# Kernel tuning notes

Hardware: AMD Instinct MI355X
Metric: run time of the kernel (lower is better)

The kernel has to match this reference:

```python
import jax, jax.numpy as jnp
import numpy as np

N = 50000
E = 400000
D = 128

def _linear(v, W, b):
    return v @ W + b

def setup_inputs() -> dict:
    key = jax.random.key(0)
    ks = jax.random.split(key, 24)
    inp = {
        'h': jax.random.normal(ks[0], (N, D), jnp.float32),
        'x': jax.random.normal(ks[1], (N, 3), jnp.float32),
        'src': jax.random.randint(ks[2], (E,), 0, N, jnp.int32),
        'dst': jax.random.randint(ks[3], (E,), 0, N, jnp.int32),
        'distances': jax.random.uniform(ks[4], (E,), jnp.float32),
        'bpp_bias': jax.random.uniform(ks[5], (E,), jnp.float32),
        'msa_bias': jax.random.uniform(ks[6], (E,), jnp.float32),
        'chem_bias': jax.random.uniform(ks[7], (E,), jnp.float32),
        'relative_offset': jax.random.normal(ks[8], (E,), jnp.float32),
        'chain_break_mask': jax.random.uniform(ks[9], (E,), jnp.float32),
    }
    s = 0.05
    # weights stored [in, out] (transpose of torch Linear)
    inp['msg_W1'] = jax.random.normal(ks[10], (2 * D + 6, D), jnp.float32) * s
    inp['msg_b1'] = jnp.zeros((D,), jnp.float32)
    inp['msg_W2'] = jax.random.normal(ks[11], (D, D), jnp.float32) * s
    inp['msg_b2'] = jnp.zeros((D,), jnp.float32)
    inp['h_W1'] = jax.random.normal(ks[12], (2 * D, D), jnp.float32) * s
    inp['h_b1'] = jnp.zeros((D,), jnp.float32)
    inp['h_W2'] = jax.random.normal(ks[13], (D, D), jnp.float32) * s
    inp['h_b2'] = jnp.zeros((D,), jnp.float32)
    inp['c_W1'] = jax.random.normal(ks[14], (D, D), jnp.float32) * s
    inp['c_b1'] = jnp.zeros((D,), jnp.float32)
    inp['c_W2'] = jax.random.normal(ks[15], (D, 1), jnp.float32) * s
    inp['c_b2'] = jnp.zeros((1,), jnp.float32)
    return inp

def reference(h, x, src, dst, distances, bpp_bias, msa_bias, chem_bias,
              relative_offset, chain_break_mask,
              msg_W1, msg_b1, msg_W2, msg_b2,
              h_W1, h_b1, h_W2, h_b2,
              c_W1, c_b1, c_W2, c_b2):
    n = h.shape[0]
    h_src = h[src]                      # [E, D]
    h_dst = h[dst]                      # [E, D]
    diff = x[src] - x[dst]              # [E, 3]
    dist2 = (distances * distances)[:, None]
    feat = jnp.concatenate([
        h_src, h_dst, dist2,
        bpp_bias[:, None], msa_bias[:, None], chem_bias[:, None],
        relative_offset[:, None], chain_break_mask[:, None]], axis=-1)  # [E, 2D+6]
    m_ij = jax.nn.silu(_linear(jax.nn.silu(_linear(feat, msg_W1, msg_b1)), msg_W2, msg_b2))  # [E, D]
    counts = jax.ops.segment_sum(jnp.ones((src.shape[0],), h.dtype), src, num_segments=n)[:, None]  # [N,1]
    denom = jnp.maximum(counts, 1.0)
    m_i = jax.ops.segment_sum(m_ij, src, num_segments=n) / denom      # [N, D]
    h_out = h + _linear(jax.nn.silu(_linear(jnp.concatenate([h, m_i], -1), h_W1, h_b1)), h_W2, h_b2)
    coef = jnp.tanh(_linear(jax.nn.silu(_linear(m_ij, c_W1, c_b1)), c_W2, c_b2))  # [E, 1]
    delta = jax.ops.segment_sum(diff * coef, src, num_segments=n) / denom          # [N, 3]
    x_out = x + delta
    return h_out, x_out
```

## Files before the change

kernel.cpp:

```cpp
#include <hip/hip_runtime.h>
#include <hip/hip_bf16.h>

typedef short bf16x8 __attribute__((ext_vector_type(8)));
typedef float f32x16 __attribute__((ext_vector_type(16)));
typedef int   i32x4v __attribute__((ext_vector_type(4)));
typedef unsigned u32;

#define MFMA32(a,b,c) __builtin_amdgcn_mfma_f32_32x32x16_bf16((a),(b),(c),0,0,0)

__device__ __forceinline__ u32 pkbf(float x, float y) {
  union { u32 u; __hip_bfloat16 h[2]; } t;
  t.h[0] = __float2bfloat16(x);
  t.h[1] = __float2bfloat16(y);
  return t.u;
}
__device__ __forceinline__ float bf2f(u32 lo16) {
  union { u32 u; float f; } t; t.u = lo16 << 16; return t.f;
}
__device__ __forceinline__ float silu_f(float v) { return v / (1.f + __expf(-v)); }
__device__ __forceinline__ float tanh_f(float v) {
  float e = __expf(2.f * fabsf(v));
  float t = 1.f - 2.f / (e + 1.f);
  return copysignf(t, v);
}

template<int NT>
__device__ __forceinline__ void stage_w128t(const float* __restrict__ W, short* wA, int tid) {
  for (int p = tid; p < 8192; p += NT) {
    int j = p & 127;
    int k = (p >> 7) << 1;
    u32 u = pkbf(W[k * 128 + j], W[k * 128 + 128 + j]);
    int off = j * 256 + (((k >> 3) ^ (j & 15)) << 4) + ((k & 7) << 1);
    *(u32*)((char*)wA + off) = u;
  }
}
__device__ __forceinline__ bf16x8 ldsA(const short* wA, int j, int kbase) {
  int off = j * 256 + (((kbase >> 3) ^ (j & 15)) << 4);
  return __builtin_bit_cast(bf16x8, *(const i32x4v*)((const char*)wA + off));
}

__device__ __forceinline__ void row_chunks(u32 p0, u32 p1, u32 p2, u32 p3,
                                           u32 p4, u32 p5, u32 p6, u32 p7,
                                           int hi, char* rowptr, int jm) {
  u32 x0 = (u32)__shfl_xor((int)(hi ? p0 : p4), 32);
  u32 x1 = (u32)__shfl_xor((int)(hi ? p1 : p5), 32);
  u32 x2 = (u32)__shfl_xor((int)(hi ? p2 : p6), 32);
  u32 x3 = (u32)__shfl_xor((int)(hi ? p3 : p7), 32);
  i32x4v c0, c1;
  if (hi) {
    c0[0] = (int)x0; c0[1] = (int)x1; c0[2] = (int)p4; c0[3] = (int)p5;
    c1[0] = (int)x2; c1[1] = (int)x3; c1[2] = (int)p6; c1[3] = (int)p7;
  } else {
    c0[0] = (int)p0; c0[1] = (int)p1; c0[2] = (int)x0; c0[3] = (int)x1;
    c1[0] = (int)p2; c1[1] = (int)p3; c1[2] = (int)x2; c1[3] = (int)x3;
  }
  *(i32x4v*)(rowptr + jm * 64 + hi * 32)      = c0;
  *(i32x4v*)(rowptr + jm * 64 + hi * 32 + 16) = c1;
}

__device__ __forceinline__ void trans_store1(const f32x16& a, const float* bias, int hi,
                                             char* rowptr, bool va, int jm) {
  float v[16];
  #pragma unroll
  for (int r = 0; r < 16; ++r) {
    int rowloc = (r & 3) + 8 * (r >> 2) + 4 * hi;
    v[r] = silu_f(a[r] + bias[jm * 32 + rowloc]);
  }
  u32 p0 = pkbf(v[0], v[1]),  p1 = pkbf(v[2], v[3]);
  u32 p2 = pkbf(v[4], v[5]),  p3 = pkbf(v[6], v[7]);
  u32 p4 = pkbf(v[8], v[9]),  p5 = pkbf(v[10], v[11]);
  u32 p6 = pkbf(v[12], v[13]), p7 = pkbf(v[14], v[15]);
  if (va) row_chunks(p0, p1, p2, p3, p4, p5, p6, p7, hi, rowptr, jm);
}

__device__ __forceinline__ void trans_frag1(const f32x16& a, const float* bias, int hi,
                                            i32x4v* fr, char* rowptr, bool va, int jm) {
  float v[16];
  #pragma unroll
  for (int r = 0; r < 16; ++r) {
    int rowloc = (r & 3) + 8 * (r >> 2) + 4 * hi;
    v[r] = silu_f(a[r] + bias[jm * 32 + rowloc]);
  }
  u32 p0 = pkbf(v[0], v[1]),  p1 = pkbf(v[2], v[3]);
  u32 p2 = pkbf(v[4], v[5]),  p3 = pkbf(v[6], v[7]);
  u32 p4 = pkbf(v[8], v[9]),  p5 = pkbf(v[10], v[11]);
  u32 p6 = pkbf(v[12], v[13]), p7 = pkbf(v[14], v[15]);
  {
    u32 g1 = (u32)__shfl_xor((int)(hi ? p0 : p2), 32);
    u32 g2 = (u32)__shfl_xor((int)(hi ? p1 : p3), 32);
    i32x4v w;
    w[0] = hi ? (int)g1 : (int)p0;
    w[1] = hi ? (int)g2 : (int)p1;
    w[2] = hi ? (int)p2 : (int)g1;
    w[3] = hi ? (int)p3 : (int)g2;
    fr[jm * 2] = w;
    u32 g1b = (u32)__shfl_xor((int)(hi ? p4 : p6), 32);
    u32 g2b = (u32)__shfl_xor((int)(hi ? p5 : p7), 32);
    i32x4v w2;
    w2[0] = hi ? (int)g1b : (int)p4;
    w2[1] = hi ? (int)g2b : (int)p5;
    w2[2] = hi ? (int)p6 : (int)g1b;
    w2[3] = hi ? (int)p7 : (int)g2b;
    fr[jm * 2 + 1] = w2;
  }
  if (va) row_chunks(p0, p1, p2, p3, p4, p5, p6, p7, hi, rowptr, jm);
}


__global__ void kconv(const float* __restrict__ h, char* __restrict__ hbf, int total16) {
  int i = blockIdx.x * 256 + threadIdx.x;
  if (i >= total16) return;
  const float4* h4 = (const float4*)h;
  float4 a = h4[(size_t)i * 2], b = h4[(size_t)i * 2 + 1];
  i32x4v w;
  w[0] = (int)pkbf(a.x, a.y); w[1] = (int)pkbf(a.z, a.w);
  w[2] = (int)pkbf(b.x, b.y); w[3] = (int)pkbf(b.z, b.w);
  *(i32x4v*)(hbf + (size_t)i * 16) = w;
}

__global__ void khist(const int* __restrict__ src, int* __restrict__ cnt, int E) {
  int e = blockIdx.x * 256 + threadIdx.x;
  if (e < E) atomicAdd(&cnt[src[e]], 1);
}

__global__ void kscan1(const int* __restrict__ cnt, int* __restrict__ part,
                       int* __restrict__ bsums, int N) {
  __shared__ int sh[1024];
  int tid = threadIdx.x, i = blockIdx.x * 1024 + tid;
  int v = (i < N) ? cnt[i] : 0;
  sh[tid] = v; __syncthreads();
  for (int off = 1; off < 1024; off <<= 1) {
    int t = (tid >= off) ? sh[tid - off] : 0;
    __syncthreads();
    sh[tid] += t;
    __syncthreads();
  }
  if (i < N) part[i] = sh[tid] - v;
  if (tid == 1023) bsums[blockIdx.x] = sh[1023];
}

__global__ void kscan2(int* __restrict__ bsums, int nb) {
  __shared__ int sh[64];
  int tid = threadIdx.x;
  int v = (tid < nb) ? bsums[tid] : 0;
  sh[tid] = v; __syncthreads();
  for (int off = 1; off < 64; off <<= 1) {
    int t = (tid >= off) ? sh[tid - off] : 0;
    __syncthreads();
    sh[tid] += t;
    __syncthreads();
  }
  if (tid < nb) bsums[tid] = sh[tid] - v;
}

__global__ void kscan3(const int* __restrict__ bsums, int* __restrict__ part,
                       int* __restrict__ head, int N) {
  int i = blockIdx.x * 1024 + threadIdx.x;
  if (i < N) {
    int v = part[i] + bsums[blockIdx.x];
    part[i] = v;
    head[i] = v;
  }
}

__global__ void kscatter(const int* __restrict__ src, const int* __restrict__ dst,
                         const float* __restrict__ dist, const float* __restrict__ bpp,
                         const float* __restrict__ msa, const float* __restrict__ chem,
                         const float* __restrict__ rel, const float* __restrict__ cbm,
                         int* __restrict__ head, int* __restrict__ rec, int E) {
  int e = blockIdx.x * 256 + threadIdx.x;
  if (e >= E) return;
  int s = src[e];
  int p = atomicAdd(&head[s], 1);
  float q = dist[e];
  i32x4v a;
  a[0] = s;
  a[1] = dst[e];
  a[2] = (int)pkbf(q * q, bpp[e]);
  a[3] = (int)pkbf(msa[e], chem[e]);
  *(i32x4v*)(rec + (size_t)p * 8) = a;
  rec[(size_t)p * 8 + 4] = (int)pkbf(rel[e], cbm[e]);
}

__global__ __launch_bounds__(512, 2)
void kedgeA(const char* __restrict__ hbf, const int* __restrict__ rec,
            const float* __restrict__ mW1, const float* __restrict__ mb1,
            char* __restrict__ t1, int E)
{
  __shared__ short wA0[16384], wA1[16384];
  __shared__ short wE[2048];
  __shared__ float sb1[128];

  const int tid = threadIdx.x, wid = tid >> 6, lane = tid & 63;
  const int col = lane & 31, hi = lane >> 5;

  stage_w128t<512>(mW1, wA0, tid);
  stage_w128t<512>(mW1 + 16384, wA1, tid);
  for (int p = tid; p < 2048; p += 512) {
    int j = p >> 4, kk = p & 15;
    float w = (kk < 6) ? mW1[(256 + kk) * 128 + j] : 0.f;
    wE[j * 16 + kk] = (short)(pkbf(w, 0.f) & 0xffffu);
  }
  if (tid < 128) sb1[tid] = mb1[tid];
  __syncthreads();

  const int T = (E + 31) / 32;
  const int stride = gridDim.x * 8;
  int t = blockIdx.x * 8 + wid;
  if (t >= T) return;

  int p = t * 32 + col;
  int pc = p < E ? p : E - 1;
  i32x4v ra = *(const i32x4v*)(rec + (size_t)pc * 8);
  int ev2 = rec[(size_t)pc * 8 + 4];

  while (t < T) {
    bool va = p < E;
    int s = ra[0], d = ra[1];

    i32x4v bs[8], bd[8];
    #pragma unroll
    for (int kc = 0; kc < 8; ++kc)
      bs[kc] = *(const i32x4v*)(hbf + (size_t)s * 256 + kc * 32 + hi * 16);
    #pragma unroll
    for (int kc = 0; kc < 8; ++kc)
      bd[kc] = *(const i32x4v*)(hbf + (size_t)d * 256 + kc * 32 + hi * 16);

    int tn = t + stride;
    int pn = tn * 32 + col;
    int pcn = pn < E ? pn : E - 1;
    i32x4v nra = *(const i32x4v*)(rec + (size_t)pcn * 8);
    int nev2 = rec[(size_t)pcn * 8 + 4];

    char* rowptr = t1 + (size_t)p * 256;
    #pragma unroll
    for (int g = 0; g < 2; ++g) {
      f32x16 acc2[2];
      #pragma unroll
      for (int j2 = 0; j2 < 2; ++j2)
        #pragma unroll
        for (int r = 0; r < 16; ++r) acc2[j2][r] = 0.f;

      #pragma unroll
      for (int kc = 0; kc < 8; ++kc) {
        bf16x8 bb = __builtin_bit_cast(bf16x8, bs[kc]);
        #pragma unroll
        for (int j2 = 0; j2 < 2; ++j2)
          acc2[j2] = MFMA32(ldsA(wA0, (g * 2 + j2) * 32 + col, kc * 16 + hi * 8), bb, acc2[j2]);
      }
      #pragma unroll
      for (int kc = 0; kc < 8; ++kc) {
        bf16x8 bb = __builtin_bit_cast(bf16x8, bd[kc]);
        #pragma unroll
        for (int j2 = 0; j2 < 2; ++j2)
          acc2[j2] = MFMA32(ldsA(wA1, (g * 2 + j2) * 32 + col, kc * 16 + hi * 8), bb, acc2[j2]);
      }
      {
        i32x4v ev;
        ev[0] = hi ? 0 : ra[2];
        ev[1] = hi ? 0 : ra[3];
        ev[2] = hi ? 0 : ev2;
        ev[3] = 0;
        bf16x8 be = __builtin_bit_cast(bf16x8, ev);
        #pragma unroll
        for (int j2 = 0; j2 < 2; ++j2) {
          bf16x8 af = __builtin_bit_cast(bf16x8,
              *(const i32x4v*)((const char*)wE + ((g * 2 + j2) * 32 + col) * 32 + hi * 16));
          acc2[j2] = MFMA32(af, be, acc2[j2]);
        }
      }
      #pragma unroll
      for (int j2 = 0; j2 < 2; ++j2)
        trans_store1(acc2[j2], sb1, hi, rowptr, va, g * 2 + j2);
    }

    t = tn; p = pn; ra = nra; ev2 = nev2;
  }
}

__global__ __launch_bounds__(512, 2)
void kedgeB(char* buf,
            const float* __restrict__ mW2, const float* __restrict__ mb2,
            const float* __restrict__ cW1, const float* __restrict__ cb1,
            const float* __restrict__ cW2v, const float* __restrict__ cb2,
            float* __restrict__ coef, int E)
{
  __shared__ short wA2[16384], wA3[16384];
  __shared__ float sb2[128], scb1[128], scw2[128];
  __shared__ float scb2v[1];

  const int tid = threadIdx.x, wid = tid >> 6, lane = tid & 63;
  const int col = lane & 31, hi = lane >> 5;

  stage_w128t<512>(mW2, wA2, tid);
  stage_w128t<512>(cW1, wA3, tid);
  if (tid < 128) {
    sb2[tid] = mb2[tid]; scb1[tid] = cb1[tid]; scw2[tid] = cW2v[tid];
  }
  if (tid == 0) scb2v[0] = cb2[0];
  __syncthreads();

  const int T = (E + 31) / 32;
  const int stride = gridDim.x * 8;
  for (int t = blockIdx.x * 8 + wid; t < T; t += stride) {
    int p = t * 32 + col;
    bool va = p < E;
    int pc = va ? p : E - 1;

    i32x4v b[8];
    #pragma unroll
    for (int kc = 0; kc < 8; ++kc)
      b[kc] = *(const i32x4v*)(buf + (size_t)pc * 256 + kc * 32 + hi * 16);

    char* rowptr = buf + (size_t)p * 256;
    i32x4v fr[8];
    #pragma unroll
    for (int g = 0; g < 2; ++g) {
      f32x16 acc2[2];
      #pragma unroll
      for (int j2 = 0; j2 < 2; ++j2)
        #pragma unroll
        for (int r = 0; r < 16; ++r) acc2[j2][r] = 0.f;
      #pragma unroll
      for (int kc = 0; kc < 8; ++kc) {
        bf16x8 bb = __builtin_bit_cast(bf16x8, b[kc]);
        #pragma unroll
        for (int j2 = 0; j2 < 2; ++j2)
          acc2[j2] = MFMA32(ldsA(wA2, (g * 2 + j2) * 32 + col, kc * 16 + hi * 8), bb, acc2[j2]);
      }
      #pragma unroll
      for (int j2 = 0; j2 < 2; ++j2)
        trans_frag1(acc2[j2], sb2, hi, fr, rowptr, va, g * 2 + j2);
    }

    float part = 0.f;
    #pragma unroll
    for (int g = 0; g < 2; ++g) {
      f32x16 acc2[2];
      #pragma unroll
      for (int j2 = 0; j2 < 2; ++j2)
        #pragma unroll
        for (int r = 0; r < 16; ++r) acc2[j2][r] = 0.f;
      #pragma unroll
      for (int kc = 0; kc < 8; ++kc) {
        bf16x8 bb = __builtin_bit_cast(bf16x8, fr[kc]);
        #pragma unroll
        for (int j2 = 0; j2 < 2; ++j2)
          acc2[j2] = MFMA32(ldsA(wA3, (g * 2 + j2) * 32 + col, kc * 16 + hi * 8), bb, acc2[j2]);
      }
      #pragma unroll
      for (int j2 = 0; j2 < 2; ++j2) {
        int jm = g * 2 + j2;
        #pragma unroll
        for (int r = 0; r < 16; ++r) {
          int rowloc = (r & 3) + 8 * (r >> 2) + 4 * hi;
          part += silu_f(acc2[j2][r] + scb1[jm * 32 + rowloc]) * scw2[jm * 32 + rowloc];
        }
      }
    }
    part += __shfl_xor(part, 32);
    float cf = tanh_f(part + scb2v[0]);
    if (va && hi == 0) coef[p] = cf;
  }
}

__global__ __launch_bounds__(256)
void kagg(const char* __restrict__ m_ij, const int* __restrict__ row_start,
          const int* __restrict__ cnt, const float* __restrict__ coef,
          const int* __restrict__ rec, const float* __restrict__ x,
          char* __restrict__ mibf, float* __restrict__ outX, int N)
{
  int n = blockIdx.x * 16 + (threadIdx.x >> 4);
  int t = threadIdx.x & 15;
  if (n >= N) return;
  int st = row_start[n], c = cnt[n];
  float a[8] = {0.f, 0.f, 0.f, 0.f, 0.f, 0.f, 0.f, 0.f};
  for (int k = 0; k < c; ++k) {
    i32x4v u = *(const i32x4v*)(m_ij + (size_t)(st + k) * 256 + t * 16);
    #pragma unroll
    for (int q = 0; q < 4; ++q) {
      u32 w = (u32)u[q];
      a[q * 2]     += bf2f(w & 0xffffu);
      a[q * 2 + 1] += bf2f(w >> 16);
    }
  }
  float inv = 1.f / fmaxf((float)c, 1.f);
  i32x4v o;
  #pragma unroll
  for (int q = 0; q < 4; ++q) o[q] = (int)pkbf(a[q * 2] * inv, a[q * 2 + 1] * inv);
  *(i32x4v*)(mibf + (size_t)n * 256 + t * 16) = o;
  if (t == 0) {
    float x0 = x[(size_t)n * 3], x1 = x[(size_t)n * 3 + 1], x2 = x[(size_t)n * 3 + 2];
    float dx = 0.f, dy = 0.f, dz = 0.f;
    for (int k = 0; k < c; ++k) {
      float cf = coef[st + k];
      int dn = rec[(size_t)(st + k) * 8 + 1];
      dx += (x0 - x[(size_t)dn * 3])     * cf;
      dy += (x1 - x[(size_t)dn * 3 + 1]) * cf;
      dz += (x2 - x[(size_t)dn * 3 + 2]) * cf;
    }
    outX[(size_t)n * 3]     = x0 + dx * inv;
    outX[(size_t)n * 3 + 1] = x1 + dy * inv;
    outX[(size_t)n * 3 + 2] = x2 + dz * inv;
  }
}

__global__ __launch_bounds__(512, 2)
void knode1(const char* __restrict__ hbf, const char* __restrict__ mibf,
            const float* __restrict__ hW1, const float* __restrict__ hb1,
            char* __restrict__ t1h, int N)
{
  __shared__ short wA0[16384], wA1[16384];
  __shared__ float sb1[128];
  const int tid = threadIdx.x, wid = tid >> 6, lane = tid & 63;
  const int col = lane & 31, hi = lane >> 5;
  stage_w128t<512>(hW1, wA0, tid);
  stage_w128t<512>(hW1 + 16384, wA1, tid);
  if (tid < 128) sb1[tid] = hb1[tid];
  __syncthreads();

  int T = (N + 31) / 32;
  int t = blockIdx.x * 8 + wid;
  if (t >= T) return;
  int n = t * 32 + col;
  bool va = n < N;
  int nc = va ? n : N - 1;

  i32x4v bh[8], bm[8];
  #pragma unroll
  for (int kc = 0; kc < 8; ++kc)
    bh[kc] = *(const i32x4v*)(hbf + (size_t)nc * 256 + kc * 32 + hi * 16);
  #pragma unroll
  for (int kc = 0; kc < 8; ++kc)
    bm[kc] = *(const i32x4v*)(mibf + (size_t)nc * 256 + kc * 32 + hi * 16);

  char* rowptr = t1h + (size_t)n * 256;
  #pragma unroll
  for (int g = 0; g < 2; ++g) {
    f32x16 acc2[2];
    #pragma unroll
    for (int j2 = 0; j2 < 2; ++j2)
      #pragma unroll
      for (int r = 0; r < 16; ++r) acc2[j2][r] = 0.f;
    #pragma unroll
    for (int kc = 0; kc < 8; ++kc) {
      bf16x8 bb = __builtin_bit_cast(bf16x8, bh[kc]);
      #pragma unroll
      for (int j2 = 0; j2 < 2; ++j2)
        acc2[j2] = MFMA32(ldsA(wA0, (g * 2 + j2) * 32 + col, kc * 16 + hi * 8), bb, acc2[j2]);
    }
    #pragma unroll
    for (int kc = 0; kc < 8; ++kc) {
      bf16x8 bb = __builtin_bit_cast(bf16x8, bm[kc]);
      #pragma unroll
      for (int j2 = 0; j2 < 2; ++j2)
        acc2[j2] = MFMA32(ldsA(wA1, (g * 2 + j2) * 32 + col, kc * 16 + hi * 8), bb, acc2[j2]);
    }
    #pragma unroll
    for (int j2 = 0; j2 < 2; ++j2)
      trans_store1(acc2[j2], sb1, hi, rowptr, va, g * 2 + j2);
  }
}

__global__ __launch_bounds__(512, 2)
void knode2(const char* __restrict__ t1h, const float* __restrict__ hW2,
            const float* __restrict__ hb2, const float* __restrict__ h,
            float* __restrict__ outH, int N)
{
  __shared__ short wA0[16384];
  __shared__ float sb2[128];
  const int tid = threadIdx.x, wid = tid >> 6, lane = tid & 63;
  const int col = lane & 31, hi = lane >> 5;
  stage_w128t<512>(hW2, wA0, tid);
  if (tid < 128) sb2[tid] = hb2[tid];
  __syncthreads();

  int T = (N + 31) / 32;
  int t = blockIdx.x * 8 + wid;
  if (t >= T) return;
  int n = t * 32 + col;
  bool va = n < N;
  int nc = va ? n : N - 1;

  i32x4v b[8];
  #pragma unroll
  for (int kc = 0; kc < 8; ++kc)
    b[kc] = *(const i32x4v*)(t1h + (size_t)nc * 256 + kc * 32 + hi * 16);

  const float4* h4 = (const float4*)h;
  #pragma unroll
  for (int g = 0; g < 2; ++g) {
    f32x16 acc2[2];
    #pragma unroll
    for (int j2 = 0; j2 < 2; ++j2)
      #pragma unroll
      for (int r = 0; r < 16; ++r) acc2[j2][r] = 0.f;
    #pragma unroll
    for (int kc = 0; kc < 8; ++kc) {
      bf16x8 bb = __builtin_bit_cast(bf16x8, b[kc]);
      #pragma unroll
      for (int j2 = 0; j2 < 2; ++j2)
        acc2[j2] = MFMA32(ldsA(wA0, (g * 2 + j2) * 32 + col, kc * 16 + hi * 8), bb, acc2[j2]);
    }
    #pragma unroll
    for (int j2 = 0; j2 < 2; ++j2) {
      int jm = g * 2 + j2;
      #pragma unroll
      for (int rq = 0; rq < 4; ++rq) {
        int j0 = jm * 32 + rq * 8 + hi * 4;
        float4 hv = h4[(size_t)nc * 32 + (j0 >> 2)];
        float4 o;
        o.x = hv.x + acc2[j2][rq * 4 + 0] + sb2[j0 + 0];
        o.y = hv.y + acc2[j2][rq * 4 + 1] + sb2[j0 + 1];
        o.z = hv.z + acc2[j2][rq * 4 + 2] + sb2[j0 + 2];
        o.w = hv.w + acc2[j2][rq * 4 + 3] + sb2[j0 + 3];
        if (va) ((float4*)outH)[(size_t)nc * 32 + (j0 >> 2)] = o;
      }
    }
  }
}


extern "C" void kernel_launch(void* const* d_in, const int* in_sizes, int n_in,
                              void* d_out, int out_size, void* d_ws, size_t ws_size,
                              hipStream_t stream) {
  const float* h    = (const float*)d_in[0];
  const float* x    = (const float*)d_in[1];
  const int*   src  = (const int*)d_in[2];
  const int*   dst  = (const int*)d_in[3];
  const float* dist = (const float*)d_in[4];
  const float* bpp  = (const float*)d_in[5];
  const float* msa  = (const float*)d_in[6];
  const float* chem = (const float*)d_in[7];
  const float* rel  = (const float*)d_in[8];
  const float* cbm  = (const float*)d_in[9];
  const float* mW1  = (const float*)d_in[10];
  const float* mb1  = (const float*)d_in[11];
  const float* mW2  = (const float*)d_in[12];
  const float* mb2  = (const float*)d_in[13];
  const float* hW1  = (const float*)d_in[14];
  const float* hb1  = (const float*)d_in[15];
  const float* hW2  = (const float*)d_in[16];
  const float* hb2  = (const float*)d_in[17];
  const float* cW1  = (const float*)d_in[18];
  const float* cb1  = (const float*)d_in[19];
  const float* cW2  = (const float*)d_in[20];
  const float* cb2  = (const float*)d_in[21];

  int N = in_sizes[0] / 128;
  int E = in_sizes[2];

  size_t off = 0;
  auto A = [&](size_t b) { size_t o = off; off += (b + 255) & ~(size_t)255; return o; };
  size_t o_cnt  = A((size_t)N * 4);
  size_t o_rs   = A((size_t)N * 4);
  size_t o_head = A((size_t)N * 4);
  size_t o_rec  = A((size_t)E * 32);
  size_t o_coef = A((size_t)E * 4);
  size_t o_bs   = A(1024);
  size_t o_hbf  = A((size_t)N * 256);
  size_t o_mibf = A((size_t)N * 256);
  size_t o_big  = A((size_t)E * 256);

  char* W = (char*)d_ws;
  int*   cnt32 = (int*)(W + o_cnt);
  int*   rs    = (int*)(W + o_rs);
  int*   head  = (int*)(W + o_head);
  int*   rec   = (int*)(W + o_rec);
  float* coef  = (float*)(W + o_coef);
  int*   bsums = (int*)(W + o_bs);
  char*  hbf   = W + o_hbf;
  char*  mibf  = W + o_mibf;
  char*  big   = W + o_big;

  hipMemsetAsync(cnt32, 0, (size_t)N * 4, stream);
  kconv<<<(N * 16 + 255) / 256, 256, 0, stream>>>(h, hbf, N * 16);
  khist<<<(E + 255) / 256, 256, 0, stream>>>(src, cnt32, E);
  int nb = (N + 1023) / 1024;
  kscan1<<<nb, 1024, 0, stream>>>(cnt32, rs, bsums, N);
  kscan2<<<1, 64, 0, stream>>>(bsums, nb);
  kscan3<<<nb, 1024, 0, stream>>>(bsums, rs, head, N);
  kscatter<<<(E + 255) / 256, 256, 0, stream>>>(src, dst, dist, bpp, msa, chem, rel, cbm,
                                                head, rec, E);
  kedgeA<<<512, 512, 0, stream>>>(hbf, rec, mW1, mb1, big, E);
  kedgeB<<<512, 512, 0, stream>>>(big, mW2, mb2, cW1, cb1, cW2, cb2, coef, E);
  kagg<<<(N + 15) / 16, 256, 0, stream>>>(big, rs, cnt32, coef, rec, x,
                                          mibf, (float*)d_out + (size_t)N * 128, N);
  int tb = ((N + 31) / 32 + 7) / 8;
  knode1<<<tb, 512, 0, stream>>>(hbf, mibf, hW1, hb1, big, N);
  knode2<<<tb, 512, 0, stream>>>(big, hW2, hb2, h, (float*)d_out, N);
}
```

Baseline: 669.5 us.

## Store intermediate activations in tiled fragment-major layout for coalesced access

Intermediate bf16 activation buffers (edge hidden t1, m_ij, node hidden t1h) switch from row-major 256-byte rows to 32-row tiles of 8 KB, where each lane writes and reads contiguous 16-byte chunks at lane*16 offsets. Both the producer stores and the consumer MFMA fragment loads become fully coalesced, 1 KB-contiguous wave accesses instead of strided row accesses. The segment-reduce kernel is rewritten to index the tiled layout, which makes its per-edge reads more scattered. The buffer is padded by one tile so the tail tile is fully addressable.

```diff
diff --git a/kernel.cpp b/kernel.cpp
--- a/kernel.cpp
+++ b/kernel.cpp
@@ -39,9 +39,10 @@
   return __builtin_bit_cast(bf16x8, *(const i32x4v*)((const char*)wA + off));
 }
 
-__device__ __forceinline__ void row_chunks(u32 p0, u32 p1, u32 p2, u32 p3,
-                                           u32 p4, u32 p5, u32 p6, u32 p7,
-                                           int hi, char* rowptr, int jm) {
+
+__device__ __forceinline__ void tile_chunks(u32 p0, u32 p1, u32 p2, u32 p3,
+                                            u32 p4, u32 p5, u32 p6, u32 p7,
+                                            int hi, int lane, char* tb, int jm) {
   u32 x0 = (u32)__shfl_xor((int)(hi ? p0 : p4), 32);
   u32 x1 = (u32)__shfl_xor((int)(hi ? p1 : p5), 32);
   u32 x2 = (u32)__shfl_xor((int)(hi ? p2 : p6), 32);
@@ -54,12 +55,16 @@
     c0[0] = (int)p0; c0[1] = (int)p1; c0[2] = (int)x0; c0[3] = (int)x1;
     c1[0] = (int)p2; c1[1] = (int)p3; c1[2] = (int)x2; c1[3] = (int)x3;
   }
-  *(i32x4v*)(rowptr + jm * 64 + hi * 32)      = c0;
-  *(i32x4v*)(rowptr + jm * 64 + hi * 32 + 16) = c1;
+  *(i32x4v*)(tb + (jm * 2 + 0) * 1024 + lane * 16) = c0;
+  *(i32x4v*)(tb + (jm * 2 + 1) * 1024 + lane * 16) = c1;
+}
+
+__device__ __forceinline__ i32x4v tile_load(const char* tb, int kc, int hi, int col) {
+  return *(const i32x4v*)(tb + ((kc >> 1) * 2 + hi) * 1024 + ((kc & 1) * 32 + col) * 16);
 }
 
 __device__ __forceinline__ void trans_store1(const f32x16& a, const float* bias, int hi,
-                                             char* rowptr, bool va, int jm) {
+                                             int lane, char* tb, bool va, int jm) {
   float v[16];
   #pragma unroll
   for (int r = 0; r < 16; ++r) {
@@ -70,11 +75,11 @@
   u32 p2 = pkbf(v[4], v[5]),  p3 = pkbf(v[6], v[7]);
   u32 p4 = pkbf(v[8], v[9]),  p5 = pkbf(v[10], v[11]);
   u32 p6 = pkbf(v[12], v[13]), p7 = pkbf(v[14], v[15]);
-  if (va) row_chunks(p0, p1, p2, p3, p4, p5, p6, p7, hi, rowptr, jm);
+  if (va) tile_chunks(p0, p1, p2, p3, p4, p5, p6, p7, hi, lane, tb, jm);
 }
 
 __device__ __forceinline__ void trans_frag1(const f32x16& a, const float* bias, int hi,
-                                            i32x4v* fr, char* rowptr, bool va, int jm) {
+                                            int lane, i32x4v* fr, char* tb, bool va, int jm) {
   float v[16];
   #pragma unroll
   for (int r = 0; r < 16; ++r) {
@@ -103,7 +108,7 @@
     w2[3] = hi ? (int)p7 : (int)g2b;
     fr[jm * 2 + 1] = w2;
   }
-  if (va) row_chunks(p0, p1, p2, p3, p4, p5, p6, p7, hi, rowptr, jm);
+  if (va) tile_chunks(p0, p1, p2, p3, p4, p5, p6, p7, hi, lane, tb, jm);
 }
 
 
@@ -232,7 +237,7 @@
     i32x4v nra = *(const i32x4v*)(rec + (size_t)pcn * 8);
     int nev2 = rec[(size_t)pcn * 8 + 4];
 
-    char* rowptr = t1 + (size_t)p * 256;
+    char* tb = t1 + (size_t)t * 8192;
     #pragma unroll
     for (int g = 0; g < 2; ++g) {
       f32x16 acc2[2];
@@ -271,7 +276,7 @@
       }
       #pragma unroll
       for (int j2 = 0; j2 < 2; ++j2)
-        trans_store1(acc2[j2], sb1, hi, rowptr, va, g * 2 + j2);
+        trans_store1(acc2[j2], sb1, hi, lane, tb, va, g * 2 + j2);
     }
 
     t = tn; p = pn; ra = nra; ev2 = nev2;
@@ -305,14 +310,13 @@
   for (int t = blockIdx.x * 8 + wid; t < T; t += stride) {
     int p = t * 32 + col;
     bool va = p < E;
-    int pc = va ? p : E - 1;
+    char* tb = buf + (size_t)t * 8192;
 
     i32x4v b[8];
     #pragma unroll
     for (int kc = 0; kc < 8; ++kc)
-      b[kc] = *(const i32x4v*)(buf + (size_t)pc * 256 + kc * 32 + hi * 16);
-
-    char* rowptr = buf + (size_t)p * 256;
+      b[kc] = tile_load(tb, kc, hi, col);
+
     i32x4v fr[8];
     #pragma unroll
     for (int g = 0; g < 2; ++g) {
@@ -330,7 +334,7 @@
       }
       #pragma unroll
       for (int j2 = 0; j2 < 2; ++j2)
-        trans_frag1(acc2[j2], sb2, hi, fr, rowptr, va, g * 2 + j2);
+        trans_frag1(acc2[j2], sb2, hi, lane, fr, tb, va, g * 2 + j2);
     }
 
     float part = 0.f;
@@ -374,9 +378,11 @@
   int t = threadIdx.x & 15;
   if (n >= N) return;
   int st = row_start[n], c = cnt[n];
+  int toff = ((t >> 2) * 2 + (t & 1)) * 1024 + (((t >> 1) & 1) * 32) * 16;
   float a[8] = {0.f, 0.f, 0.f, 0.f, 0.f, 0.f, 0.f, 0.f};
   for (int k = 0; k < c; ++k) {
-    i32x4v u = *(const i32x4v*)(m_ij + (size_t)(st + k) * 256 + t * 16);
+    int sk = st + k;
+    i32x4v u = *(const i32x4v*)(m_ij + (size_t)(sk >> 5) * 8192 + toff + (sk & 31) * 16);
     #pragma unroll
     for (int q = 0; q < 4; ++q) {
       u32 w = (u32)u[q];
@@ -434,7 +440,7 @@
   for (int kc = 0; kc < 8; ++kc)
     bm[kc] = *(const i32x4v*)(mibf + (size_t)nc * 256 + kc * 32 + hi * 16);
 
-  char* rowptr = t1h + (size_t)n * 256;
+  char* tb = t1h + (size_t)t * 8192;
   #pragma unroll
   for (int g = 0; g < 2; ++g) {
     f32x16 acc2[2];
@@ -458,7 +464,7 @@
     }
     #pragma unroll
     for (int j2 = 0; j2 < 2; ++j2)
-      trans_store1(acc2[j2], sb1, hi, rowptr, va, g * 2 + j2);
+      trans_store1(acc2[j2], sb1, hi, lane, tb, va, g * 2 + j2);
   }
 }
 
@@ -482,10 +488,11 @@
   bool va = n < N;
   int nc = va ? n : N - 1;
 
+  const char* tb = t1h + (size_t)t * 8192;
   i32x4v b[8];
   #pragma unroll
   for (int kc = 0; kc < 8; ++kc)
-    b[kc] = *(const i32x4v*)(t1h + (size_t)nc * 256 + kc * 32 + hi * 16);
+    b[kc] = tile_load(tb, kc, hi, col);
 
   const float4* h4 = (const float4*)h;
   #pragma unroll
@@ -560,7 +567,7 @@
   size_t o_bs   = A(1024);
   size_t o_hbf  = A((size_t)N * 256);
   size_t o_mibf = A((size_t)N * 256);
-  size_t o_big  = A((size_t)E * 256);
+  size_t o_big  = A(((size_t)E + 32) * 256);
 
   char* W = (char*)d_ws;
   int*   cnt32 = (int*)(W + o_cnt);
```

Result: slower. 738.8 us (+10.4%).

## Software-pipeline next-tile gathers in edge kernels to overlap with MFMA

Applied to the files above, without the earlier changes.

Both edge kernels now prefetch the next tile's input rows into registers while the current tile's MFMAs run. In kedgeA the group loop is unrolled by hand so the next src/dst h rows can be loaded as soon as each register set is consumed. In kedgeB the next m_ij tile is loaded after the first GEMM, overlapping with the coef GEMM. This hides gather latency but raises register pressure, which could reduce occupancy or cause spills, and the last iteration issues redundant clamped loads.

```diff
diff --git a/kernel.cpp b/kernel.cpp
--- a/kernel.cpp
+++ b/kernel.cpp
@@ -214,17 +214,19 @@
   i32x4v ra = *(const i32x4v*)(rec + (size_t)pc * 8);
   int ev2 = rec[(size_t)pc * 8 + 4];
 
+  i32x4v bs[8], bd[8];
+  {
+    int s = ra[0], d = ra[1];
+    #pragma unroll
+    for (int kc = 0; kc < 8; ++kc)
+      bs[kc] = *(const i32x4v*)(hbf + (size_t)s * 256 + kc * 32 + hi * 16);
+    #pragma unroll
+    for (int kc = 0; kc < 8; ++kc)
+      bd[kc] = *(const i32x4v*)(hbf + (size_t)d * 256 + kc * 32 + hi * 16);
+  }
+
   while (t < T) {
     bool va = p < E;
-    int s = ra[0], d = ra[1];
-
-    i32x4v bs[8], bd[8];
-    #pragma unroll
-    for (int kc = 0; kc < 8; ++kc)
-      bs[kc] = *(const i32x4v*)(hbf + (size_t)s * 256 + kc * 32 + hi * 16);
-    #pragma unroll
-    for (int kc = 0; kc < 8; ++kc)
-      bd[kc] = *(const i32x4v*)(hbf + (size_t)d * 256 + kc * 32 + hi * 16);
 
     int tn = t + stride;
     int pn = tn * 32 + col;
@@ -233,27 +235,26 @@
     int nev2 = rec[(size_t)pcn * 8 + 4];
 
     char* rowptr = t1 + (size_t)p * 256;
-    #pragma unroll
-    for (int g = 0; g < 2; ++g) {
+
+    {
       f32x16 acc2[2];
       #pragma unroll
       for (int j2 = 0; j2 < 2; ++j2)
         #pragma unroll
         for (int r = 0; r < 16; ++r) acc2[j2][r] = 0.f;
-
       #pragma unroll
       for (int kc = 0; kc < 8; ++kc) {
         bf16x8 bb = __builtin_bit_cast(bf16x8, bs[kc]);
         #pragma unroll
         for (int j2 = 0; j2 < 2; ++j2)
-          acc2[j2] = MFMA32(ldsA(wA0, (g * 2 + j2) * 32 + col, kc * 16 + hi * 8), bb, acc2[j2]);
+          acc2[j2] = MFMA32(ldsA(wA0, j2 * 32 + col, kc * 16 + hi * 8), bb, acc2[j2]);
       }
       #pragma unroll
       for (int kc = 0; kc < 8; ++kc) {
         bf16x8 bb = __builtin_bit_cast(bf16x8, bd[kc]);
         #pragma unroll
         for (int j2 = 0; j2 < 2; ++j2)
-          acc2[j2] = MFMA32(ldsA(wA1, (g * 2 + j2) * 32 + col, kc * 16 + hi * 8), bb, acc2[j2]);
+          acc2[j2] = MFMA32(ldsA(wA1, j2 * 32 + col, kc * 16 + hi * 8), bb, acc2[j2]);
       }
       {
         i32x4v ev;
@@ -265,13 +266,62 @@
         #pragma unroll
         for (int j2 = 0; j2 < 2; ++j2) {
           bf16x8 af = __builtin_bit_cast(bf16x8,
-              *(const i32x4v*)((const char*)wE + ((g * 2 + j2) * 32 + col) * 32 + hi * 16));
+              *(const i32x4v*)((const char*)wE + (j2 * 32 + col) * 32 + hi * 16));
           acc2[j2] = MFMA32(af, be, acc2[j2]);
         }
       }
-      #pragma unroll
-      for (int j2 = 0; j2 < 2; ++j2)
-        trans_store1(acc2[j2], sb1, hi, rowptr, va, g * 2 + j2);
+      trans_store1(acc2[0], sb1, hi, rowptr, va, 0);
+      trans_store1(acc2[1], sb1, hi, rowptr, va, 1);
+    }
+
+    {
+      f32x16 acc2[2];
+      #pragma unroll
+      for (int j2 = 0; j2 < 2; ++j2)
+        #pragma unroll
+        for (int r = 0; r < 16; ++r) acc2[j2][r] = 0.f;
+      #pragma unroll
+      for (int kc = 0; kc < 8; ++kc) {
+        bf16x8 bb = __builtin_bit_cast(bf16x8, bs[kc]);
+        #pragma unroll
+        for (int j2 = 0; j2 < 2; ++j2)
+          acc2[j2] = MFMA32(ldsA(wA0, (2 + j2) * 32 + col, kc * 16 + hi * 8), bb, acc2[j2]);
+      }
+      {
+        int sn = nra[0];
+        #pragma unroll
+        for (int kc = 0; kc < 8; ++kc)
+          bs[kc] = *(const i32x4v*)(hbf + (size_t)sn * 256 + kc * 32 + hi * 16);
+      }
+      #pragma unroll
+      for (int kc = 0; kc < 8; ++kc) {
+        bf16x8 bb = __builtin_bit_cast(bf16x8, bd[kc]);
+        #pragma unroll
+        for (int j2 = 0; j2 < 2; ++j2)
+          acc2[j2] = MFMA32(ldsA(wA1, (2 + j2) * 32 + col, kc * 16 + hi * 8), bb, acc2[j2]);
+      }
+      {
+        int dn = nra[1];
+        #pragma unroll
+        for (int kc = 0; kc < 8; ++kc)
+          bd[kc] = *(const i32x4v*)(hbf + (size_t)dn * 256 + kc * 32 + hi * 16);
+      }
+      {
+        i32x4v ev;
+        ev[0] = hi ? 0 : ra[2];
+        ev[1] = hi ? 0 : ra[3];
+        ev[2] = hi ? 0 : ev2;
+        ev[3] = 0;
+        bf16x8 be = __builtin_bit_cast(bf16x8, ev);
+        #pragma unroll
+        for (int j2 = 0; j2 < 2; ++j2) {
+          bf16x8 af = __builtin_bit_cast(bf16x8,
+              *(const i32x4v*)((const char*)wE + ((2 + j2) * 32 + col) * 32 + hi * 16));
+          acc2[j2] = MFMA32(af, be, acc2[j2]);
+        }
+      }
+      trans_store1(acc2[0], sb1, hi, rowptr, va, 2);
+      trans_store1(acc2[1], sb1, hi, rowptr, va, 3);
     }
 
     t = tn; p = pn; ra = nra; ev2 = nev2;
@@ -302,17 +352,22 @@
 
   const int T = (E + 31) / 32;
   const int stride = gridDim.x * 8;
-  for (int t = blockIdx.x * 8 + wid; t < T; t += stride) {
-    int p = t * 32 + col;
-    bool va = p < E;
-    int pc = va ? p : E - 1;
-
-    i32x4v b[8];
+  int t = blockIdx.x * 8 + wid;
+  if (t >= T) return;
+  int p = t * 32 + col;
+
+  i32x4v b[8];
+  {
+    int pc = p < E ? p : E - 1;
     #pragma unroll
     for (int kc = 0; kc < 8; ++kc)
       b[kc] = *(const i32x4v*)(buf + (size_t)pc * 256 + kc * 32 + hi * 16);
-
+  }
+
+  while (t < T) {
+    bool va = p < E;
     char* rowptr = buf + (size_t)p * 256;
+
     i32x4v fr[8];
     #pragma unroll
     for (int g = 0; g < 2; ++g) {
@@ -331,6 +386,15 @@
       #pragma unroll
       for (int j2 = 0; j2 < 2; ++j2)
         trans_frag1(acc2[j2], sb2, hi, fr, rowptr, va, g * 2 + j2);
+    }
+
+    int tn = t + stride;
+    int pn2 = tn * 32 + col;
+    {
+      int pcn = pn2 < E ? pn2 : E - 1;
+      #pragma unroll
+      for (int kc = 0; kc < 8; ++kc)
+        b[kc] = *(const i32x4v*)(buf + (size_t)pcn * 256 + kc * 32 + hi * 16);
     }
 
     float part = 0.f;
@@ -361,6 +425,8 @@
     part += __shfl_xor(part, 32);
     float cf = tanh_f(part + scb2v[0]);
     if (va && hi == 0) coef[p] = cf;
+
+    t = tn; p = pn2;
   }
 }
 
```

Result: slower. 705.1 us (+5.3%).

## Fuse edge MLP layers into one kernel keeping hidden activations in registers

Applied to the files above, without the earlier changes.

Merges the first message-MLP layer kernel with the second-layer/coef kernel so the hidden activation for each edge tile goes from MFMA accumulators into register fragments and is never written to global memory. Only the final m_ij is stored. It also prefetches the next tile's source-node row and the current dst row while MFMAs run, which overlaps gathers with compute. The cost is LDS use of about 132KB per block, which limits occupancy to one block per CU (the grid is cut to 256), plus higher register pressure from four accumulators.

```diff
diff --git a/kernel.cpp b/kernel.cpp
--- a/kernel.cpp
+++ b/kernel.cpp
@@ -183,25 +183,35 @@
 }
 
 __global__ __launch_bounds__(512, 2)
-void kedgeA(const char* __restrict__ hbf, const int* __restrict__ rec,
-            const float* __restrict__ mW1, const float* __restrict__ mb1,
-            char* __restrict__ t1, int E)
+void kedgeAB(const char* __restrict__ hbf, const int* __restrict__ rec,
+             const float* __restrict__ mW1, const float* __restrict__ mb1,
+             const float* __restrict__ mW2, const float* __restrict__ mb2,
+             const float* __restrict__ cW1, const float* __restrict__ cb1,
+             const float* __restrict__ cW2v, const float* __restrict__ cb2,
+             char* __restrict__ m_ij, float* __restrict__ coef, int E)
 {
-  __shared__ short wA0[16384], wA1[16384];
+  __shared__ short wA0[16384], wA1[16384], wA2[16384], wA3[16384];
   __shared__ short wE[2048];
-  __shared__ float sb1[128];
+  __shared__ float sb1[128], sb2[128], scb1[128], scw2[128];
+  __shared__ float scb2v[1];
 
   const int tid = threadIdx.x, wid = tid >> 6, lane = tid & 63;
   const int col = lane & 31, hi = lane >> 5;
 
   stage_w128t<512>(mW1, wA0, tid);
   stage_w128t<512>(mW1 + 16384, wA1, tid);
+  stage_w128t<512>(mW2, wA2, tid);
+  stage_w128t<512>(cW1, wA3, tid);
   for (int p = tid; p < 2048; p += 512) {
     int j = p >> 4, kk = p & 15;
     float w = (kk < 6) ? mW1[(256 + kk) * 128 + j] : 0.f;
     wE[j * 16 + kk] = (short)(pkbf(w, 0.f) & 0xffffu);
   }
-  if (tid < 128) sb1[tid] = mb1[tid];
+  if (tid < 128) {
+    sb1[tid] = mb1[tid]; sb2[tid] = mb2[tid];
+    scb1[tid] = cb1[tid]; scw2[tid] = cW2v[tid];
+  }
+  if (tid == 0) scb2v[0] = cb2[0];
   __syncthreads();
 
   const int T = (E + 31) / 32;
@@ -214,17 +224,13 @@
   i32x4v ra = *(const i32x4v*)(rec + (size_t)pc * 8);
   int ev2 = rec[(size_t)pc * 8 + 4];
 
+  i32x4v b[8];
+  #pragma unroll
+  for (int kc = 0; kc < 8; ++kc)
+    b[kc] = *(const i32x4v*)(hbf + (size_t)ra[0] * 256 + kc * 32 + hi * 16);
+
   while (t < T) {
     bool va = p < E;
-    int s = ra[0], d = ra[1];
-
-    i32x4v bs[8], bd[8];
-    #pragma unroll
-    for (int kc = 0; kc < 8; ++kc)
-      bs[kc] = *(const i32x4v*)(hbf + (size_t)s * 256 + kc * 32 + hi * 16);
-    #pragma unroll
-    for (int kc = 0; kc < 8; ++kc)
-      bd[kc] = *(const i32x4v*)(hbf + (size_t)d * 256 + kc * 32 + hi * 16);
 
     int tn = t + stride;
     int pn = tn * 32 + col;
@@ -232,7 +238,49 @@
     i32x4v nra = *(const i32x4v*)(rec + (size_t)pcn * 8);
     int nev2 = rec[(size_t)pcn * 8 + 4];
 
-    char* rowptr = t1 + (size_t)p * 256;
+    f32x16 acc[4];
+    #pragma unroll
+    for (int jm = 0; jm < 4; ++jm)
+      #pragma unroll
+      for (int r = 0; r < 16; ++r) acc[jm][r] = 0.f;
+
+    #pragma unroll
+    for (int kc = 0; kc < 8; ++kc) {
+      bf16x8 bb = __builtin_bit_cast(bf16x8, b[kc]);
+      b[kc] = *(const i32x4v*)(hbf + (size_t)ra[1] * 256 + kc * 32 + hi * 16);
+      #pragma unroll
+      for (int jm = 0; jm < 4; ++jm)
+        acc[jm] = MFMA32(ldsA(wA0, jm * 32 + col, kc * 16 + hi * 8), bb, acc[jm]);
+    }
+    #pragma unroll
+    for (int kc = 0; kc < 8; ++kc) {
+      bf16x8 bb = __builtin_bit_cast(bf16x8, b[kc]);
+      #pragma unroll
+      for (int jm = 0; jm < 4; ++jm)
+        acc[jm] = MFMA32(ldsA(wA1, jm * 32 + col, kc * 16 + hi * 8), bb, acc[jm]);
+    }
+    {
+      i32x4v ev;
+      ev[0] = hi ? 0 : ra[2];
+      ev[1] = hi ? 0 : ra[3];
+      ev[2] = hi ? 0 : ev2;
+      ev[3] = 0;
+      bf16x8 be = __builtin_bit_cast(bf16x8, ev);
+      #pragma unroll
+      for (int jm = 0; jm < 4; ++jm) {
+        bf16x8 af = __builtin_bit_cast(bf16x8,
+            *(const i32x4v*)((const char*)wE + (jm * 32 + col) * 32 + hi * 16));
+        acc[jm] = MFMA32(af, be, acc[jm]);
+      }
+    }
+
+    i32x4v fr1[8];
+    #pragma unroll
+    for (int jm = 0; jm < 4; ++jm)
+      trans_frag1(acc[jm], sb1, hi, fr1, nullptr, false, jm);
+
+    char* rowptr = m_ij + (size_t)p * 256;
+    i32x4v fr2[8];
     #pragma unroll
     for (int g = 0; g < 2; ++g) {
       f32x16 acc2[2];
@@ -240,98 +288,21 @@
       for (int j2 = 0; j2 < 2; ++j2)
         #pragma unroll
         for (int r = 0; r < 16; ++r) acc2[j2][r] = 0.f;
-
       #pragma unroll
       for (int kc = 0; kc < 8; ++kc) {
-        bf16x8 bb = __builtin_bit_cast(bf16x8, bs[kc]);
-        #pragma unroll
-        for (int j2 = 0; j2 < 2; ++j2)
-          acc2[j2] = MFMA32(ldsA(wA0, (g * 2 + j2) * 32 + col, kc * 16 + hi * 8), bb, acc2[j2]);
-      }
-      #pragma unroll
-      for (int kc = 0; kc < 8; ++kc) {
-        bf16x8 bb = __builtin_bit_cast(bf16x8, bd[kc]);
-        #pragma unroll
-        for (int j2 = 0; j2 < 2; ++j2)
-          acc2[j2] = MFMA32(ldsA(wA1, (g * 2 + j2) * 32 + col, kc * 16 + hi * 8), bb, acc2[j2]);
-      }
-      {
-        i32x4v ev;
-        ev[0] = hi ? 0 : ra[2];
-        ev[1] = hi ? 0 : ra[3];
-        ev[2] = hi ? 0 : ev2;
-        ev[3] = 0;
-        bf16x8 be = __builtin_bit_cast(bf16x8, ev);
-        #pragma unroll
-        for (int j2 = 0; j2 < 2; ++j2) {
-          bf16x8 af = __builtin_bit_cast(bf16x8,
-              *(const i32x4v*)((const char*)wE + ((g * 2 + j2) * 32 + col) * 32 + hi * 16));
-          acc2[j2] = MFMA32(af, be, acc2[j2]);
-        }
-      }
-      #pragma unroll
-      for (int j2 = 0; j2 < 2; ++j2)
-        trans_store1(acc2[j2], sb1, hi, rowptr, va, g * 2 + j2);
-    }
-
-    t = tn; p = pn; ra = nra; ev2 = nev2;
-  }
-}
-
-__global__ __launch_bounds__(512, 2)
-void kedgeB(char* buf,
-            const float* __restrict__ mW2, const float* __restrict__ mb2,
-            const float* __restrict__ cW1, const float* __restrict__ cb1,
-            const float* __restrict__ cW2v, const float* __restrict__ cb2,
-            float* __restrict__ coef, int E)
-{
-  __shared__ short wA2[16384], wA3[16384];
-  __shared__ float sb2[128], scb1[128], scw2[128];
-  __shared__ float scb2v[1];
-
-  const int tid = threadIdx.x, wid = tid >> 6, lane = tid & 63;
-  const int col = lane & 31, hi = lane >> 5;
-
-  stage_w128t<512>(mW2, wA2, tid);
-  stage_w128t<512>(cW1, wA3, tid);
-  if (tid < 128) {
-    sb2[tid] = mb2[tid]; scb1[tid] = cb1[tid]; scw2[tid] = cW2v[tid];
-  }
-  if (tid == 0) scb2v[0] = cb2[0];
-  __syncthreads();
-
-  const int T = (E + 31) / 32;
-  const int stride = gridDim.x * 8;
-  for (int t = blockIdx.x * 8 + wid; t < T; t += stride) {
-    int p = t * 32 + col;
-    bool va = p < E;
-    int pc = va ? p : E - 1;
-
-    i32x4v b[8];
-    #pragma unroll
-    for (int kc = 0; kc < 8; ++kc)
-      b[kc] = *(const i32x4v*)(buf + (size_t)pc * 256 + kc * 32 + hi * 16);
-
-    char* rowptr = buf + (size_t)p * 256;
-    i32x4v fr[8];
-    #pragma unroll
-    for (int g = 0; g < 2; ++g) {
-      f32x16 acc2[2];
-      #pragma unroll
-      for (int j2 = 0; j2 < 2; ++j2)
-        #pragma unroll
-        for (int r = 0; r < 16; ++r) acc2[j2][r] = 0.f;
-      #pragma unroll
-      for (int kc = 0; kc < 8; ++kc) {
-        bf16x8 bb = __builtin_bit_cast(bf16x8, b[kc]);
+        bf16x8 bb = __builtin_bit_cast(bf16x8, fr1[kc]);
         #pragma unroll
         for (int j2 = 0; j2 < 2; ++j2)
           acc2[j2] = MFMA32(ldsA(wA2, (g * 2 + j2) * 32 + col, kc * 16 + hi * 8), bb, acc2[j2]);
       }
       #pragma unroll
       for (int j2 = 0; j2 < 2; ++j2)
-        trans_frag1(acc2[j2], sb2, hi, fr, rowptr, va, g * 2 + j2);
-    }
+        trans_frag1(acc2[j2], sb2, hi, fr2, rowptr, va, g * 2 + j2);
+    }
+
+    #pragma unroll
+    for (int kc = 0; kc < 8; ++kc)
+      b[kc] = *(const i32x4v*)(hbf + (size_t)nra[0] * 256 + kc * 32 + hi * 16);
 
     float part = 0.f;
     #pragma unroll
@@ -343,7 +314,7 @@
         for (int r = 0; r < 16; ++r) acc2[j2][r] = 0.f;
       #pragma unroll
       for (int kc = 0; kc < 8; ++kc) {
-        bf16x8 bb = __builtin_bit_cast(bf16x8, fr[kc]);
+        bf16x8 bb = __builtin_bit_cast(bf16x8, fr2[kc]);
         #pragma unroll
         for (int j2 = 0; j2 < 2; ++j2)
           acc2[j2] = MFMA32(ldsA(wA3, (g * 2 + j2) * 32 + col, kc * 16 + hi * 8), bb, acc2[j2]);
@@ -361,6 +332,8 @@
     part += __shfl_xor(part, 32);
     float cf = tanh_f(part + scb2v[0]);
     if (va && hi == 0) coef[p] = cf;
+
+    t = tn; p = pn; ra = nra; ev2 = nev2;
   }
 }
 
@@ -582,8 +555,8 @@
   kscan3<<<nb, 1024, 0, stream>>>(bsums, rs, head, N);
   kscatter<<<(E + 255) / 256, 256, 0, stream>>>(src, dst, dist, bpp, msa, chem, rel, cbm,
                                                 head, rec, E);
-  kedgeA<<<512, 512, 0, stream>>>(hbf, rec, mW1, mb1, big, E);
-  kedgeB<<<512, 512, 0, stream>>>(big, mW2, mb2, cW1, cb1, cW2, cb2, coef, E);
+  kedgeAB<<<256, 512, 0, stream>>>(hbf, rec, mW1, mb1, mW2, mb2, cW1, cb1, cW2, cb2,
+                                   big, coef, E);
   kagg<<<(N + 15) / 16, 256, 0, stream>>>(big, rs, cnt32, coef, rec, x,
                                           mibf, (float*)d_out + (size_t)N * 128, N);
   int tb = ((N + 31) / 32 + 7) / 8;
```

Result: slower. 995.6 us (+48.7%).
